# Kernel optimization log

Hardware: AMD Instinct MI355X
Metric: run time of the kernel (lower is better)

## Reference

```python
import jax, jax.numpy as jnp
import numpy as np

G, N, E = 8, 10000, 160000
D_IN, D_H, D_OUT = 300, 256, 128
EPS = 1e-5


def setup_inputs() -> dict:
    key = jax.random.key(0)
    ks = jax.random.split(key, 4)
    x = jax.random.normal(ks[0], (G, N, D_IN), dtype=jnp.float32)
    edge_index = jax.random.randint(ks[1], (G, 2, E), 0, N)
    W1 = jax.random.normal(ks[2], (D_IN, D_H), dtype=jnp.float32) * (1.0 / np.sqrt(D_IN))
    b1 = jnp.zeros((D_H,), jnp.float32)
    g1 = jnp.ones((D_H,), jnp.float32)
    be1 = jnp.zeros((D_H,), jnp.float32)
    W2 = jax.random.normal(ks[3], (D_H, D_OUT), dtype=jnp.float32) * (1.0 / np.sqrt(D_H))
    b2 = jnp.zeros((D_OUT,), jnp.float32)
    g2 = jnp.ones((D_OUT,), jnp.float32)
    be2 = jnp.zeros((D_OUT,), jnp.float32)
    return dict(x=x, edge_index=edge_index, W1=W1, b1=b1, g1=g1, be1=be1,
                W2=W2, b2=b2, g2=g2, be2=be2)


def _gcn_conv(x, src, dst, W, b):
    # PyG GCNConv: h = xW; add self-loops; sym-normalized aggregation; + bias
    h = x @ W                                   # [N, F_out]
    deg = jnp.ones((N,), h.dtype).at[dst].add(1.0)  # in-degree + self-loop
    dinv = jax.lax.rsqrt(deg)                   # deg >= 1 always
    coef = dinv[src] * dinv[dst]                # [E]
    agg = jax.ops.segment_sum(h[src] * coef[:, None], dst, num_segments=N)
    agg = agg + h * (dinv * dinv)[:, None]      # self-loop term
    return agg + b


def _layernorm(x, g, b):
    mu = jnp.mean(x, axis=-1, keepdims=True)
    var = jnp.mean(jnp.square(x - mu), axis=-1, keepdims=True)
    return (x - mu) * jax.lax.rsqrt(var + EPS) * g + b


def _forward_one(xg, eg, W1, b1, g1, be1, W2, b2, g2, be2):
    src, dst = eg[0], eg[1]
    h = jax.nn.relu(_gcn_conv(xg, src, dst, W1, b1))
    h = _layernorm(h, g1, be1)
    h = _gcn_conv(h, src, dst, W2, b2)
    return _layernorm(h, g2, be2)


def reference(x, edge_index, W1, b1, g1, be1, W2, b2, g2, be2):
    f = jax.vmap(lambda xg, eg: _forward_one(xg, eg, W1, b1, g1, be1, W2, b2, g2, be2))
    return f(x, edge_index)  # [G, N, D_OUT]
```

## Files before the change

### kernel.cpp

```cpp
#include <hip/hip_runtime.h>
#include <hip/hip_bf16.h>

#define GG   8
#define NN   10000
#define EE   160000
#define DIN  300
#define KP1  320
#define DH   256
#define DOUT 128
#define LN_EPS 1e-5f

typedef short bf16x8 __attribute__((ext_vector_type(8)));
typedef float f32x4  __attribute__((ext_vector_type(4)));
typedef ushort u16x8 __attribute__((ext_vector_type(8)));

__device__ inline float bf2f(ushort u) {
    union { unsigned int i; float f; } x;
    x.i = ((unsigned int)u) << 16;
    return x.f;
}
__device__ inline ushort f2b(float f) {
    union { float f; unsigned int u; } x;
    x.f = f;
    unsigned int u = x.u;
    return (ushort)((u + 0x7fffu + ((u >> 16) & 1u)) >> 16);
}
__device__ inline short bcvt(float f) {
    __hip_bfloat16 h = __float2bfloat16(f);
    return *reinterpret_cast<short*>(&h);
}

__global__ __launch_bounds__(256) void k_util(const float* __restrict__ W1,
                                              const float* __restrict__ W2,
                                              ushort* __restrict__ w1t,
                                              ushort* __restrict__ w2t,
                                              int* __restrict__ cnt) {
    int i = blockIdx.x * blockDim.x + threadIdx.x;
    if (i < GG * NN) cnt[i] = 0;
    if (i < DH * KP1) {
        int n = i / KP1, k = i % KP1;
        w1t[i] = (k < DIN) ? f2b(W1[(size_t)k * DH + n]) : 0;
    }
    if (i < DOUT * DH) {
        int n = i / DH, k = i % DH;
        w2t[i] = f2b(W2[(size_t)k * DOUT + n]);
    }
}

__global__ __launch_bounds__(256) void k_count(const int* __restrict__ ei,
                                               int* __restrict__ cnt,
                                               int* __restrict__ slot) {
    int bid = blockIdx.x;
    int g = bid & 7;
    int e = (bid >> 3) * 256 + threadIdx.x;
    int dst = ei[(size_t)g * 2 * EE + EE + e];
    slot[(size_t)g * EE + e] = atomicAdd(&cnt[g * NN + dst], 1);
}

__global__ void k_scan(const int* __restrict__ cnt, int* __restrict__ rowptr,
                       float* __restrict__ dinv) {
    int g = blockIdx.x;
    int t = threadIdx.x;
    const int per = (NN + 255) / 256;
    __shared__ int sums[256];
    __shared__ int offs[257];
    int base = t * per;
    int s = 0;
    for (int i = 0; i < per; i++) {
        int n = base + i;
        if (n < NN) s += cnt[g * NN + n];
    }
    sums[t] = s;
    __syncthreads();
    if (t == 0) {
        int acc = 0;
        for (int i = 0; i < 256; i++) { offs[i] = acc; acc += sums[i]; }
        offs[256] = acc;
    }
    __syncthreads();
    int run = offs[t];
    for (int i = 0; i < per; i++) {
        int n = base + i;
        if (n < NN) {
            int c = cnt[g * NN + n];
            rowptr[g * (NN + 1) + n] = run;
            dinv[g * NN + n] = 1.0f / sqrtf(1.0f + (float)c);
            run += c;
        }
    }
    if (t == 255) rowptr[g * (NN + 1) + NN] = offs[256];
}

__global__ __launch_bounds__(256) void k_fill(const int* __restrict__ ei,
                                              const int* __restrict__ rowptr,
                                              const int* __restrict__ slot,
                                              const float* __restrict__ dinv,
                                              int2* __restrict__ edges) {
    int bid = blockIdx.x;
    int g = bid & 7;
    int e = (bid >> 3) * 256 + threadIdx.x;
    int src = ei[(size_t)g * 2 * EE + e];
    int dst = ei[(size_t)g * 2 * EE + EE + e];
    int pos = rowptr[g * (NN + 1) + dst] + slot[(size_t)g * EE + e];
    float coef = dinv[g * NN + src] * dinv[g * NN + dst];
    int2 rec;
    rec.x = src;
    rec.y = __float_as_int(coef);
    edges[(size_t)g * EE + pos] = rec;
}

__global__ __launch_bounds__(256) void k_gemm1(const float* __restrict__ x,
                                               const ushort* __restrict__ Bt,
                                               ushort* __restrict__ C) {
    __shared__ float  As[64 * 36];
    __shared__ ushort Bs[256 * 32];
    const int tid = threadIdx.x;
    const int lane = tid & 63;
    const int w = tid >> 6;
    const int wn = w;
    const int m0 = blockIdx.x * 64;

    const int fr = lane & 15;
    const int fk = (lane >> 4) * 8;
    const int fksB = fk ^ ((fr & 3) * 8);

    const int arow = tid >> 2;
    const int acol = (tid & 3) * 8;
    const float* xr = x + (size_t)(m0 + arow) * DIN;

    const int brow4 = (tid >> 2) & 3;
    const int bcol = ((tid & 3) ^ brow4) * 8;

    f32x4 acc[4][4];
#pragma unroll
    for (int i = 0; i < 4; i++)
#pragma unroll
        for (int j = 0; j < 4; j++) acc[i][j] = (f32x4){0.f, 0.f, 0.f, 0.f};

    float4 a0 = *(const float4*)(xr + min(acol, DIN - 4));
    float4 a1 = *(const float4*)(xr + min(acol + 4, DIN - 4));

    for (int k0 = 0; k0 < KP1; k0 += 32) {
        *(float4*)&As[arow * 36 + acol] = a0;
        *(float4*)&As[arow * 36 + acol + 4] = a1;
#pragma unroll
        for (int r = 0; r < 4; r++) {
            const ushort* gb = &Bt[(size_t)(r * 64 + (tid >> 2)) * KP1 + k0 + bcol];
            __builtin_amdgcn_global_load_lds(
                (const __attribute__((address_space(1))) void*)gb,
                (__attribute__((address_space(3))) void*)&Bs[(r * 64 + w * 16) * 32],
                16, 0, 0);
        }
        {
            const int kn = k0 + 32;
            a0 = *(const float4*)(xr + min(kn + acol, DIN - 4));
            a1 = *(const float4*)(xr + min(kn + acol + 4, DIN - 4));
        }
        __syncthreads();
        bf16x8 af[4], bfv[4];
#pragma unroll
        for (int i = 0; i < 4; i++) {
            const float* ap = &As[(i * 16 + fr) * 36 + fk];
            f32x4 p = *(const f32x4*)ap;
            f32x4 q = *(const f32x4*)(ap + 4);
            af[i][0] = bcvt(p[0]); af[i][1] = bcvt(p[1]);
            af[i][2] = bcvt(p[2]); af[i][3] = bcvt(p[3]);
            af[i][4] = bcvt(q[0]); af[i][5] = bcvt(q[1]);
            af[i][6] = bcvt(q[2]); af[i][7] = bcvt(q[3]);
            bfv[i] = *(const bf16x8*)&Bs[(wn * 64 + i * 16 + fr) * 32 + fksB];
        }
#pragma unroll
        for (int i = 0; i < 4; i++)
#pragma unroll
            for (int j = 0; j < 4; j++)
                acc[i][j] = __builtin_amdgcn_mfma_f32_16x16x32_bf16(af[i], bfv[j],
                                                                    acc[i][j], 0, 0, 0);
        __syncthreads();
    }

#pragma unroll
    for (int i = 0; i < 4; i++) {
        int row0 = m0 + i * 16 + (lane >> 4) * 4;
#pragma unroll
        for (int j = 0; j < 4; j++) {
            int col = wn * 64 + j * 16 + fr;
#pragma unroll
            for (int q = 0; q < 4; q++) {
                C[(size_t)(row0 + q) * DH + col] = f2b(acc[i][j][q]);
            }
        }
    }
}

template <int KPAD>
__global__ __launch_bounds__(256) void k_gemm_mfma(const ushort* __restrict__ A,
                                                   const ushort* __restrict__ Bt,
                                                   ushort* __restrict__ C, int Ntot) {
    __shared__ ushort As[64 * 32];
    __shared__ ushort Bs[128 * 32];
    const int tid = threadIdx.x;
    const int lane = tid & 63;
    const int w = tid >> 6;
    const int wm = w >> 1, wn = w & 1;
    const int m0 = blockIdx.x * 64;
    const int n0 = blockIdx.y * 128;

    const int srow = tid >> 2;
    const int scol = ((tid & 3) ^ (srow & 3)) * 8;

    const int fr = lane & 15;
    const int fk = (lane >> 4) * 8;
    const int fks = fk ^ ((fr & 3) * 8);

    f32x4 acc[2][4];
#pragma unroll
    for (int i = 0; i < 2; i++)
#pragma unroll
        for (int j = 0; j < 4; j++) acc[i][j] = (f32x4){0.f, 0.f, 0.f, 0.f};

    for (int k0 = 0; k0 < KPAD; k0 += 32) {
        {
            const ushort* ga = &A[(size_t)(m0 + srow) * KPAD + k0 + scol];
            __builtin_amdgcn_global_load_lds(
                (const __attribute__((address_space(1))) void*)ga,
                (__attribute__((address_space(3))) void*)&As[(w * 16) * 32],
                16, 0, 0);
        }
#pragma unroll
        for (int r = 0; r < 2; r++) {
            const ushort* gb = &Bt[(size_t)(n0 + r * 64 + srow) * KPAD + k0 + scol];
            __builtin_amdgcn_global_load_lds(
                (const __attribute__((address_space(1))) void*)gb,
                (__attribute__((address_space(3))) void*)&Bs[(r * 64 + w * 16) * 32],
                16, 0, 0);
        }
        __syncthreads();
        bf16x8 af[2], bfv[4];
#pragma unroll
        for (int i = 0; i < 2; i++)
            af[i]  = *(const bf16x8*)&As[(wm * 32 + i * 16 + fr) * 32 + fks];
#pragma unroll
        for (int j = 0; j < 4; j++)
            bfv[j] = *(const bf16x8*)&Bs[(wn * 64 + j * 16 + fr) * 32 + fks];
#pragma unroll
        for (int i = 0; i < 2; i++)
#pragma unroll
            for (int j = 0; j < 4; j++)
                acc[i][j] = __builtin_amdgcn_mfma_f32_16x16x32_bf16(af[i], bfv[j],
                                                                    acc[i][j], 0, 0, 0);
        __syncthreads();
    }

#pragma unroll
    for (int i = 0; i < 2; i++) {
        int row0 = m0 + wm * 32 + i * 16 + (lane >> 4) * 4;
#pragma unroll
        for (int j = 0; j < 4; j++) {
            int col = n0 + wn * 64 + j * 16 + fr;
#pragma unroll
            for (int q = 0; q < 4; q++) {
                C[(size_t)(row0 + q) * Ntot + col] = f2b(acc[i][j][q]);
            }
        }
    }
}

template <int D, bool RELU, typename OutT>
__global__ __launch_bounds__(256) void k_agg(const ushort* __restrict__ h,
                                             const int* __restrict__ rowptr,
                                             const int2* __restrict__ edges,
                                             const float* __restrict__ dinv,
                                             const float* __restrict__ bias,
                                             const float* __restrict__ gam,
                                             const float* __restrict__ bet,
                                             OutT* __restrict__ out) {
    constexpr int F = 8;
    constexpr int GL = D / F;
    constexpr int NPW = 64 / GL;
    __shared__ int2 s_rec[4][64];
    const int tid = threadIdx.x;
    const int lane = tid & 63;
    const int wv = tid >> 6;
    const int grp = lane / GL;
    const int gl = lane & (GL - 1);
    const int fb = gl * F;
    const int g = blockIdx.x & 7;
    const int n = (blockIdx.x >> 3) * (4 * NPW) + wv * NPW + grp;
    const ushort* hg = h + (size_t)g * NN * D;
    const int2* eg = edges + (size_t)g * EE;
    const int r0 = rowptr[g * (NN + 1) + n];
    const int r1 = rowptr[g * (NN + 1) + n + 1];
    const float dn = dinv[g * NN + n];
    int2* srw = &s_rec[wv][grp * GL];

    float acc[F];
#pragma unroll
    for (int i = 0; i < F; i++) acc[i] = 0.f;

    for (int base = r0; base < r1; base += GL) {
        const int c = min(GL, r1 - base);
        int2 rec;
        rec.x = 0;
        rec.y = 0;
        if (gl < c) rec = eg[base + gl];
        srw[gl] = rec;
        const int cpad = (c + 3) & ~3;
        for (int j = 0; j < cpad; j += 4) {
            const int4 ra = *(const int4*)&srw[j];
            const int4 rb = *(const int4*)&srw[j + 2];
            u16x8 v0 = *(const u16x8*)&hg[(size_t)ra.x * D + fb];
            u16x8 v1 = *(const u16x8*)&hg[(size_t)ra.z * D + fb];
            u16x8 v2 = *(const u16x8*)&hg[(size_t)rb.x * D + fb];
            u16x8 v3 = *(const u16x8*)&hg[(size_t)rb.z * D + fb];
            const float w0 = __int_as_float(ra.y);
            const float w1 = __int_as_float(ra.w);
            const float w2 = __int_as_float(rb.y);
            const float w3 = __int_as_float(rb.w);
#pragma unroll
            for (int i = 0; i < F; i++) acc[i] = fmaf(bf2f(v0[i]), w0, acc[i]);
#pragma unroll
            for (int i = 0; i < F; i++) acc[i] = fmaf(bf2f(v1[i]), w1, acc[i]);
#pragma unroll
            for (int i = 0; i < F; i++) acc[i] = fmaf(bf2f(v2[i]), w2, acc[i]);
#pragma unroll
            for (int i = 0; i < F; i++) acc[i] = fmaf(bf2f(v3[i]), w3, acc[i]);
        }
    }

    {
        const float ws = dn * dn;
        u16x8 v = *(const u16x8*)&hg[(size_t)n * D + fb];
#pragma unroll
        for (int i = 0; i < F; i++) {
            acc[i] = fmaf(bf2f(v[i]), ws, acc[i]);
            acc[i] += bias[fb + i];
            if (RELU) acc[i] = fmaxf(acc[i], 0.f);
        }
    }
    float s1 = 0.f, s2 = 0.f;
#pragma unroll
    for (int i = 0; i < F; i++) { s1 += acc[i]; s2 += acc[i] * acc[i]; }
#pragma unroll
    for (int o = GL / 2; o > 0; o >>= 1) {
        s1 += __shfl_xor(s1, o);
        s2 += __shfl_xor(s2, o);
    }
    const float mu = s1 / D;
    const float rs = rsqrtf(s2 / D - mu * mu + LN_EPS);

    if constexpr (sizeof(OutT) == 2) {
        u16x8 o;
#pragma unroll
        for (int i = 0; i < F; i++)
            o[i] = f2b((acc[i] - mu) * rs * gam[fb + i] + bet[fb + i]);
        *(u16x8*)&((ushort*)out)[((size_t)g * NN + n) * D + fb] = o;
    } else {
        float* op = &((float*)out)[((size_t)g * NN + n) * D + fb];
        float4 oa, ob;
        oa.x = (acc[0] - mu) * rs * gam[fb + 0] + bet[fb + 0];
        oa.y = (acc[1] - mu) * rs * gam[fb + 1] + bet[fb + 1];
        oa.z = (acc[2] - mu) * rs * gam[fb + 2] + bet[fb + 2];
        oa.w = (acc[3] - mu) * rs * gam[fb + 3] + bet[fb + 3];
        ob.x = (acc[4] - mu) * rs * gam[fb + 4] + bet[fb + 4];
        ob.y = (acc[5] - mu) * rs * gam[fb + 5] + bet[fb + 5];
        ob.z = (acc[6] - mu) * rs * gam[fb + 6] + bet[fb + 6];
        ob.w = (acc[7] - mu) * rs * gam[fb + 7] + bet[fb + 7];
        *(float4*)&op[0] = oa;
        *(float4*)&op[4] = ob;
    }
}

extern "C" void kernel_launch(void* const* d_in, const int* in_sizes, int n_in,
                              void* d_out, int out_size, void* d_ws, size_t ws_size,
                              hipStream_t stream) {
    const float* x   = (const float*)d_in[0];
    const int*   ei  = (const int*)d_in[1];
    const float* W1  = (const float*)d_in[2];
    const float* b1  = (const float*)d_in[3];
    const float* g1  = (const float*)d_in[4];
    const float* be1 = (const float*)d_in[5];
    const float* W2  = (const float*)d_in[6];
    const float* b2  = (const float*)d_in[7];
    const float* g2  = (const float*)d_in[8];
    const float* be2 = (const float*)d_in[9];
    float* out = (float*)d_out;

    char* w = (char*)d_ws;
    ushort* w1t  = (ushort*)w;                        w += (size_t)DH * KP1 * 2;
    ushort* w2t  = (ushort*)w;                        w += (size_t)DOUT * DH * 2;
    ushort* h1b  = (ushort*)w;                        w += (size_t)80000 * DH * 2;
    ushort* out1 = (ushort*)w;                        w += (size_t)80000 * DH * 2;
    int*   cnt    = (int*)w;                          w += (size_t)GG * NN * 4;
    int*   rowptr = (int*)w;                          w += (size_t)GG * (NN + 1) * 4 + 224;
    int*   slot   = (int*)w;                          w += (size_t)GG * EE * 4;
    float* dinv   = (float*)w;                        w += (size_t)GG * NN * 4;
    int2*  edges  = (int2*)w;
    ushort* h2b = h1b;

    k_util<<<dim3((DH * KP1 + 255) / 256), dim3(256), 0, stream>>>(W1, W2, w1t, w2t, cnt);

    k_count<<<dim3((EE / 256) * GG), dim3(256), 0, stream>>>(ei, cnt, slot);
    k_scan<<<dim3(GG), dim3(256), 0, stream>>>(cnt, rowptr, dinv);
    k_fill<<<dim3((EE / 256) * GG), dim3(256), 0, stream>>>(ei, rowptr, slot, dinv, edges);

    k_gemm1<<<dim3(80000 / 64), dim3(256), 0, stream>>>(x, w1t, h1b);

    k_agg<DH, true, ushort><<<dim3((NN / 8) * GG), dim3(256), 0, stream>>>(
        h1b, rowptr, edges, dinv, b1, g1, be1, out1);

    k_gemm_mfma<DH><<<dim3(80000 / 64, DOUT / 128), dim3(256), 0, stream>>>(out1, w2t, h2b, DOUT);

    k_agg<DOUT, false, float><<<dim3((NN / 16) * GG), dim3(256), 0, stream>>>(
        h2b, rowptr, edges, dinv, b2, g2, be2, out);
}
```

Measured before the change: 227.5 us.

## Fuse layer-1 aggregation, ReLU, LayerNorm with the second GEMM in one kernel

Replaces the separate layer-1 aggregation kernel and the second MFMA GEMM with one kernel. Each 512-thread block aggregates 16 nodes, applies bias, ReLU and LayerNorm, and stores the normalized rows in swizzled LDS. It then multiplies them by W2 with MFMA and writes h2 directly. This removes the out1 round trip through global memory and one launch. In exchange, each wave reads W2 from global memory with no LDS staging, and the blocks are larger and use more LDS.

```diff
diff --git a/kernel.cpp b/kernel.cpp
--- a/kernel.cpp
+++ b/kernel.cpp
@@ -8,6 +8,7 @@
 #define KP1  320
 #define DH   256
 #define DOUT 128
+#define MTOT 80000
 #define LN_EPS 1e-5f
 
 typedef short bf16x8 __attribute__((ext_vector_type(8)));
@@ -192,76 +193,116 @@
     }
 }
 
-template <int KPAD>
-__global__ __launch_bounds__(256) void k_gemm_mfma(const ushort* __restrict__ A,
-                                                   const ushort* __restrict__ Bt,
-                                                   ushort* __restrict__ C, int Ntot) {
-    __shared__ ushort As[64 * 32];
-    __shared__ ushort Bs[128 * 32];
+__global__ __launch_bounds__(512) void k_agg_gemm(const ushort* __restrict__ h,
+                                                  const int* __restrict__ rowptr,
+                                                  const int2* __restrict__ edges,
+                                                  const float* __restrict__ dinv,
+                                                  const float* __restrict__ bias,
+                                                  const float* __restrict__ gam,
+                                                  const float* __restrict__ bet,
+                                                  const ushort* __restrict__ w2t,
+                                                  ushort* __restrict__ h2) {
+    constexpr int F = 8, GL = 32, NPW = 2;
+    __shared__ int2 s_rec[8][64];
+    __shared__ ushort rows[16 * 256];
     const int tid = threadIdx.x;
     const int lane = tid & 63;
-    const int w = tid >> 6;
-    const int wm = w >> 1, wn = w & 1;
-    const int m0 = blockIdx.x * 64;
-    const int n0 = blockIdx.y * 128;
-
-    const int srow = tid >> 2;
-    const int scol = ((tid & 3) ^ (srow & 3)) * 8;
+    const int wv = tid >> 6;
+    const int grp = lane / GL;
+    const int gl = lane & (GL - 1);
+    const int fb = gl * F;
+    const int g = blockIdx.x & 7;
+    const int nb = (blockIdx.x >> 3) * 16;
+    const int node = wv * NPW + grp;
+    const int n = nb + node;
+    const ushort* hg = h + (size_t)g * NN * DH;
+    const int2* eg = edges + (size_t)g * EE;
+    const int r0 = rowptr[g * (NN + 1) + n];
+    const int r1 = rowptr[g * (NN + 1) + n + 1];
+    const float dn = dinv[g * NN + n];
+    int2* srw = &s_rec[wv][grp * GL];
+
+    float acc[F];
+#pragma unroll
+    for (int i = 0; i < F; i++) acc[i] = 0.f;
+
+    for (int base = r0; base < r1; base += GL) {
+        const int c = min(GL, r1 - base);
+        int2 rec;
+        rec.x = 0;
+        rec.y = 0;
+        if (gl < c) rec = eg[base + gl];
+        srw[gl] = rec;
+        const int cpad = (c + 3) & ~3;
+        for (int j = 0; j < cpad; j += 4) {
+            const int4 ra = *(const int4*)&srw[j];
+            const int4 rb = *(const int4*)&srw[j + 2];
+            u16x8 v0 = *(const u16x8*)&hg[(size_t)ra.x * DH + fb];
+            u16x8 v1 = *(const u16x8*)&hg[(size_t)ra.z * DH + fb];
+            u16x8 v2 = *(const u16x8*)&hg[(size_t)rb.x * DH + fb];
+            u16x8 v3 = *(const u16x8*)&hg[(size_t)rb.z * DH + fb];
+            const float w0 = __int_as_float(ra.y);
+            const float w1 = __int_as_float(ra.w);
+            const float w2 = __int_as_float(rb.y);
+            const float w3 = __int_as_float(rb.w);
+#pragma unroll
+            for (int i = 0; i < F; i++) acc[i] = fmaf(bf2f(v0[i]), w0, acc[i]);
+#pragma unroll
+            for (int i = 0; i < F; i++) acc[i] = fmaf(bf2f(v1[i]), w1, acc[i]);
+#pragma unroll
+            for (int i = 0; i < F; i++) acc[i] = fmaf(bf2f(v2[i]), w2, acc[i]);
+#pragma unroll
+            for (int i = 0; i < F; i++) acc[i] = fmaf(bf2f(v3[i]), w3, acc[i]);
+        }
+    }
+
+    {
+        const float ws = dn * dn;
+        u16x8 v = *(const u16x8*)&hg[(size_t)n * DH + fb];
+#pragma unroll
+        for (int i = 0; i < F; i++) {
+            acc[i] = fmaf(bf2f(v[i]), ws, acc[i]);
+            acc[i] += bias[fb + i];
+            acc[i] = fmaxf(acc[i], 0.f);
+        }
+    }
+    float s1 = 0.f, s2 = 0.f;
+#pragma unroll
+    for (int i = 0; i < F; i++) { s1 += acc[i]; s2 += acc[i] * acc[i]; }
+#pragma unroll
+    for (int o = GL / 2; o > 0; o >>= 1) {
+        s1 += __shfl_xor(s1, o);
+        s2 += __shfl_xor(s2, o);
+    }
+    const float mu = s1 / DH;
+    const float rs = rsqrtf(s2 / DH - mu * mu + LN_EPS);
+
+    {
+        u16x8 o;
+#pragma unroll
+        for (int i = 0; i < F; i++)
+            o[i] = f2b((acc[i] - mu) * rs * gam[fb + i] + bet[fb + i]);
+        const int slot = (gl & ~7) | ((gl & 7) ^ (node & 7));
+        *(u16x8*)&rows[node * 256 + slot * 8] = o;
+    }
+    __syncthreads();
 
     const int fr = lane & 15;
-    const int fk = (lane >> 4) * 8;
-    const int fks = fk ^ ((fr & 3) * 8);
-
-    f32x4 acc[2][4];
-#pragma unroll
-    for (int i = 0; i < 2; i++)
-#pragma unroll
-        for (int j = 0; j < 4; j++) acc[i][j] = (f32x4){0.f, 0.f, 0.f, 0.f};
-
-    for (int k0 = 0; k0 < KPAD; k0 += 32) {
-        {
-            const ushort* ga = &A[(size_t)(m0 + srow) * KPAD + k0 + scol];
-            __builtin_amdgcn_global_load_lds(
-                (const __attribute__((address_space(1))) void*)ga,
-                (__attribute__((address_space(3))) void*)&As[(w * 16) * 32],
-                16, 0, 0);
-        }
-#pragma unroll
-        for (int r = 0; r < 2; r++) {
-            const ushort* gb = &Bt[(size_t)(n0 + r * 64 + srow) * KPAD + k0 + scol];
-            __builtin_amdgcn_global_load_lds(
-                (const __attribute__((address_space(1))) void*)gb,
-                (__attribute__((address_space(3))) void*)&Bs[(r * 64 + w * 16) * 32],
-                16, 0, 0);
-        }
-        __syncthreads();
-        bf16x8 af[2], bfv[4];
-#pragma unroll
-        for (int i = 0; i < 2; i++)
-            af[i]  = *(const bf16x8*)&As[(wm * 32 + i * 16 + fr) * 32 + fks];
-#pragma unroll
-        for (int j = 0; j < 4; j++)
-            bfv[j] = *(const bf16x8*)&Bs[(wn * 64 + j * 16 + fr) * 32 + fks];
-#pragma unroll
-        for (int i = 0; i < 2; i++)
-#pragma unroll
-            for (int j = 0; j < 4; j++)
-                acc[i][j] = __builtin_amdgcn_mfma_f32_16x16x32_bf16(af[i], bfv[j],
-                                                                    acc[i][j], 0, 0, 0);
-        __syncthreads();
-    }
-
-#pragma unroll
-    for (int i = 0; i < 2; i++) {
-        int row0 = m0 + wm * 32 + i * 16 + (lane >> 4) * 4;
-#pragma unroll
-        for (int j = 0; j < 4; j++) {
-            int col = n0 + wn * 64 + j * 16 + fr;
-#pragma unroll
-            for (int q = 0; q < 4; q++) {
-                C[(size_t)(row0 + q) * Ntot + col] = f2b(acc[i][j][q]);
-            }
-        }
+    const int hi = lane >> 4;
+    const ushort* w2row = w2t + (size_t)(wv * 16 + fr) * DH;
+    f32x4 acc2 = (f32x4){0.f, 0.f, 0.f, 0.f};
+#pragma unroll
+    for (int kk = 0; kk < 8; kk++) {
+        const int cb = kk * 4 + hi;
+        const int slot = (cb & ~7) | ((cb & 7) ^ (fr & 7));
+        bf16x8 av = *(const bf16x8*)&rows[fr * 256 + slot * 8];
+        bf16x8 bv = *(const bf16x8*)(w2row + kk * 32 + hi * 8);
+        acc2 = __builtin_amdgcn_mfma_f32_16x16x32_bf16(av, bv, acc2, 0, 0, 0);
+    }
+#pragma unroll
+    for (int q = 0; q < 4; q++) {
+        const int rowg = g * NN + nb + hi * 4 + q;
+        h2[(size_t)rowg * DOUT + wv * 16 + fr] = f2b(acc2[q]);
     }
 }
 
@@ -388,14 +429,13 @@
     char* w = (char*)d_ws;
     ushort* w1t  = (ushort*)w;                        w += (size_t)DH * KP1 * 2;
     ushort* w2t  = (ushort*)w;                        w += (size_t)DOUT * DH * 2;
-    ushort* h1b  = (ushort*)w;                        w += (size_t)80000 * DH * 2;
-    ushort* out1 = (ushort*)w;                        w += (size_t)80000 * DH * 2;
+    ushort* h1b  = (ushort*)w;                        w += (size_t)MTOT * DH * 2;
+    ushort* h2b  = (ushort*)w;                        w += (size_t)MTOT * DH * 2;
     int*   cnt    = (int*)w;                          w += (size_t)GG * NN * 4;
     int*   rowptr = (int*)w;                          w += (size_t)GG * (NN + 1) * 4 + 224;
     int*   slot   = (int*)w;                          w += (size_t)GG * EE * 4;
     float* dinv   = (float*)w;                        w += (size_t)GG * NN * 4;
     int2*  edges  = (int2*)w;
-    ushort* h2b = h1b;
 
     k_util<<<dim3((DH * KP1 + 255) / 256), dim3(256), 0, stream>>>(W1, W2, w1t, w2t, cnt);
 
@@ -403,12 +443,10 @@
     k_scan<<<dim3(GG), dim3(256), 0, stream>>>(cnt, rowptr, dinv);
     k_fill<<<dim3((EE / 256) * GG), dim3(256), 0, stream>>>(ei, rowptr, slot, dinv, edges);
 
-    k_gemm1<<<dim3(80000 / 64), dim3(256), 0, stream>>>(x, w1t, h1b);
-
-    k_agg<DH, true, ushort><<<dim3((NN / 8) * GG), dim3(256), 0, stream>>>(
-        h1b, rowptr, edges, dinv, b1, g1, be1, out1);
-
-    k_gemm_mfma<DH><<<dim3(80000 / 64, DOUT / 128), dim3(256), 0, stream>>>(out1, w2t, h2b, DOUT);
+    k_gemm1<<<dim3(MTOT / 64), dim3(256), 0, stream>>>(x, w1t, h1b);
+
+    k_agg_gemm<<<dim3((NN / 16) * GG), dim3(512), 0, stream>>>(
+        h1b, rowptr, edges, dinv, b1, g1, be1, w2t, h2b);
 
     k_agg<DOUT, false, float><<<dim3((NN / 16) * GG), dim3(256), 0, stream>>>(
         h2b, rowptr, edges, dinv, b2, g2, be2, out);
```

Result: slower. 247.5 us (+8.8%).
